# Kernel tuning notes

Hardware: AMD Instinct MI355X
Metric: run time of the kernel (lower is better)

Reference implementation:

```python
import math
import jax, jax.numpy as jnp
import numpy as np

B, S, D = 2, 2048, 512
H = 8
DH = D // H  # 64
FF = 2048


def _uniform(key, shape, c):
    return jax.random.uniform(key, shape, jnp.float32, -c, c)


def setup_inputs() -> dict:
    key = jax.random.key(0)
    ks = jax.random.split(key, 16)
    x = jax.random.normal(ks[0], (B, S, D), jnp.float32)
    c_qkv = math.sqrt(6 / (D + DH))
    wq = _uniform(ks[1], (H, D, DH), c_qkv)
    wk = _uniform(ks[2], (H, D, DH), c_qkv)
    wv = _uniform(ks[3], (H, D, DH), c_qkv)
    bq = jnp.zeros((H, DH), jnp.float32)
    bk = jnp.zeros((H, DH), jnp.float32)
    bv = jnp.zeros((H, DH), jnp.float32)
    c_o = math.sqrt(6 / (H * DH + D))
    wo = _uniform(ks[4], (H * DH, D), c_o)  # stored as (in, out)
    bo = jnp.zeros((D,), jnp.float32)
    gamma1 = jnp.ones((D,), jnp.float32)
    beta1 = jnp.zeros((D,), jnp.float32)
    c_ff = math.sqrt(6 / (D + FF))
    w1 = _uniform(ks[5], (D, FF), c_ff)
    b1 = jnp.zeros((FF,), jnp.float32)
    w2 = _uniform(ks[6], (FF, D), c_ff)
    b2 = jnp.zeros((D,), jnp.float32)
    gamma2 = jnp.ones((D,), jnp.float32)
    beta2 = jnp.zeros((D,), jnp.float32)
    return dict(x=x, wq=wq, bq=bq, wk=wk, bk=bk, wv=wv, bv=bv, wo=wo, bo=bo,
                gamma1=gamma1, beta1=beta1, w1=w1, b1=b1, w2=w2, b2=b2,
                gamma2=gamma2, beta2=beta2)


def _layernorm(x, gamma, beta):
    # matches torch: (x - mean) / std(unbiased=False), no epsilon in denom
    mean = jnp.mean(x, axis=-1, keepdims=True)
    var = jnp.mean((x - mean) ** 2, axis=-1, keepdims=True)
    return gamma * (x - mean) / jnp.sqrt(var) + beta


def reference(x, wq, bq, wk, bk, wv, bv, wo, bo, gamma1, beta1, w1, b1, w2, b2, gamma2, beta2):
    # multi-head attention: all heads batched in one einsum (same math as the per-head loop)
    q = jnp.einsum('bsd,hde->bhse', x, wq) + bq[None, :, None, :]
    k = jnp.einsum('bsd,hde->bhse', x, wk) + bk[None, :, None, :]
    v = jnp.einsum('bsd,hde->bhse', x, wv) + bv[None, :, None, :]
    scores = jnp.einsum('bhse,bhte->bhst', q, k) / math.sqrt(DH)  # [B,H,S,S]
    attn = jax.nn.softmax(scores, axis=-1)
    y = jnp.einsum('bhst,bhte->bhse', attn, v)  # [B,H,S,DH]
    y = y.transpose(0, 2, 1, 3).reshape(B, S, H * DH)
    y = y @ wo + bo
    # residual + LN (dropout is identity in eval)
    y = _layernorm(y + x, gamma1, beta1)
    # feedforward
    f = jax.nn.relu(y @ w1 + b1) @ w2 + b2
    out = _layernorm(f + y, gamma2, beta2)
    return out
```

## Files before the change

### kernel.cpp

```cpp
#include <hip/hip_runtime.h>

typedef __bf16 bf16;
typedef __attribute__((ext_vector_type(8))) __bf16 bf16x8;
typedef __attribute__((ext_vector_type(4))) float f32x4;
typedef __attribute__((ext_vector_type(16))) float f32x16;

#define DEV __device__ __forceinline__

DEV f32x4 mfma16(bf16x8 a, bf16x8 b, f32x4 c) {
  return __builtin_amdgcn_mfma_f32_16x16x32_bf16(a, b, c, 0, 0, 0);
}
DEV f32x16 mfma32(bf16x8 a, bf16x8 b, f32x16 c) {
  return __builtin_amdgcn_mfma_f32_32x32x16_bf16(a, b, c, 0, 0, 0);
}
DEV void gll16(const bf16* g, bf16* l) {
  __builtin_amdgcn_global_load_lds(
      (const __attribute__((address_space(1))) void*)g,
      (__attribute__((address_space(3))) void*)l, 16, 0, 0);
}
DEV unsigned cvtpk(float a, float b) {
  unsigned r;
  asm("v_cvt_pk_bf16_f32 %0, %1, %2" : "=v"(r) : "v"(a), "v"(b));
  return r;
}
DEV void pl32swap(unsigned& x, unsigned& y) {
  asm("v_permlane32_swap_b32 %0, %1" : "+v"(x), "+v"(y));
}

__global__ __launch_bounds__(256) void prep_k(
    const float* __restrict__ x, const float* __restrict__ wq,
    const float* __restrict__ wk, const float* __restrict__ wv,
    const float* __restrict__ wo, const float* __restrict__ w1,
    const float* __restrict__ w2, const float* __restrict__ bq,
    const float* __restrict__ bk, const float* __restrict__ bv,
    bf16* __restrict__ xb, bf16* __restrict__ wqkvT, bf16* __restrict__ woT,
    bf16* __restrict__ w1T, bf16* __restrict__ w2T, float* __restrict__ cb) {
  const int blk = blockIdx.x, tid = threadIdx.x;
  if (blk < 1024) {
    int i = blk * 256 + tid;
    const float4* p = (const float4*)x + (size_t)i * 2;
    float4 a = p[0], b = p[1];
    bf16x8 o;
    o[0] = (bf16)a.x; o[1] = (bf16)a.y; o[2] = (bf16)a.z; o[3] = (bf16)a.w;
    o[4] = (bf16)b.x; o[5] = (bf16)b.y; o[6] = (bf16)b.z; o[7] = (bf16)b.w;
    ((bf16x8*)xb)[i] = o;
    return;
  }
  if (blk == 1792) {
    for (int i = tid; i < 1536; i += 256)
      cb[i] = i < 512 ? bq[i] : (i < 1024 ? bk[i - 512] : bv[i - 1024]);
    return;
  }
  __shared__ float tile[64][65];
  const int t = blk - 1024;
  const float* src;
  bf16* dst;
  int C, Rout, r0, c0;
  if (t < 192) {
    int mat = t / 64, rem = t % 64, head = rem >> 3, rt = rem & 7;
    src = (mat == 0 ? wq : mat == 1 ? wk : wv) + head * 32768;
    dst = wqkvT + (size_t)(mat * 8 + head) * 32768;
    C = 64; Rout = 512; r0 = rt * 64; c0 = 0;
  } else if (t < 256) {
    int t2 = t - 192;
    src = wo; dst = woT; C = 512; Rout = 512;
    r0 = (t2 >> 3) * 64; c0 = (t2 & 7) * 64;
  } else if (t < 512) {
    int t2 = t - 256;
    src = w1; dst = w1T; C = 2048; Rout = 512;
    r0 = (t2 >> 5) * 64; c0 = (t2 & 31) * 64;
  } else {
    int t2 = t - 512;
    src = w2; dst = w2T; C = 512; Rout = 2048;
    r0 = (t2 >> 3) * 64; c0 = (t2 & 7) * 64;
  }
#pragma unroll
  for (int j = 0; j < 4; ++j) {
    int e = j * 256 + tid;
    int r = e >> 4, c4 = e & 15;
    float4 f = *(const float4*)(src + (size_t)(r0 + r) * C + c0 + c4 * 4);
    tile[r][c4 * 4 + 0] = f.x;
    tile[r][c4 * 4 + 1] = f.y;
    tile[r][c4 * 4 + 2] = f.z;
    tile[r][c4 * 4 + 3] = f.w;
  }
  __syncthreads();
  const int co = tid >> 2, rr0 = (tid & 3) * 16;
  bf16x8 o0, o1;
#pragma unroll
  for (int k = 0; k < 8; ++k) o0[k] = (bf16)tile[rr0 + k][co];
#pragma unroll
  for (int k = 0; k < 8; ++k) o1[k] = (bf16)tile[rr0 + 8 + k][co];
  bf16* dp = dst + (size_t)(c0 + co) * Rout + r0 + rr0;
  *(bf16x8*)dp = o0;
  *(bf16x8*)(dp + 8) = o1;
}

__global__ __launch_bounds__(256) void vtrans_k(const bf16* __restrict__ qkv,
                                                bf16* __restrict__ vtb) {
  __shared__ bf16 tile[64 * 68];
  const int tid = threadIdx.x;
  const int s0 = blockIdx.x * 64;
  const int bh = blockIdx.y, b = bh >> 3, hh = bh & 7;
  const bf16* src = qkv + 1024 + hh * 64;
#pragma unroll
  for (int j = 0; j < 2; ++j) {
    int slot = j * 256 + tid;
    int r = slot >> 3, cc = slot & 7;
    *(bf16x8*)(tile + r * 68 + cc * 8) =
        *(const bf16x8*)(src + (size_t)(b * 2048 + s0 + r) * 1536 + cc * 8);
  }
  __syncthreads();
  const int w = tid >> 6, lane = tid & 63;
#pragma unroll
  for (int sb2 = 0; sb2 < 2; ++sb2) {
    int sb = w * 2 + sb2;
    bf16x8 v;
#pragma unroll
    for (int jj = 0; jj < 8; ++jj) v[jj] = tile[(sb * 8 + jj) * 68 + lane];
    *(bf16x8*)(vtb + (size_t)bh * 131072 + (size_t)lane * 2048 + s0 + sb * 8) = v;
  }
}

template <int EPI>
__global__ __launch_bounds__(256) void gemmN64(
    const bf16* __restrict__ A, const bf16* __restrict__ Bt,
    const float* __restrict__ bias, float* __restrict__ outf,
    bf16* __restrict__ outb, int M, int N, int K, int klen) {
  __shared__ bf16 As[128 * 64];
  __shared__ bf16 Bs[64 * 64];
  const int tid = threadIdx.x;
  const int w = tid >> 6, l = tid & 63;
  const int lh = l & 15, lg = l >> 4;
  const int m0 = blockIdx.x * 128, n0 = blockIdx.y * 64;
  const int k0 = blockIdx.z * klen;
  const int mb = (w & 1) * 64, nb = (w >> 1) * 32;
  f32x4 acc[4][2] = {};
  for (int kt = k0; kt < k0 + klen; kt += 64) {
    __syncthreads();
#pragma unroll
    for (int j = 0; j < 4; ++j) {
      int slot = j * 256 + tid;
      int r = slot >> 3, cc = slot & 7;
      int kk = kt + ((cc ^ (r & 7)) << 3);
      gll16(A + (size_t)(m0 + r) * K + kk, As + slot * 8);
    }
#pragma unroll
    for (int j = 0; j < 2; ++j) {
      int slot = j * 256 + tid;
      int r = slot >> 3, cc = slot & 7;
      int kk = kt + ((cc ^ (r & 7)) << 3);
      gll16(Bt + (size_t)(n0 + r) * K + kk, Bs + slot * 8);
    }
    __syncthreads();
#pragma unroll
    for (int kk = 0; kk < 2; ++kk) {
      bf16x8 af[4], bfr[2];
#pragma unroll
      for (int mi = 0; mi < 4; ++mi) {
        int r = mb + mi * 16 + lh;
        af[mi] = *(const bf16x8*)(As + r * 64 + (((kk * 4 + lg) ^ (r & 7)) << 3));
      }
#pragma unroll
      for (int ni = 0; ni < 2; ++ni) {
        int r = nb + ni * 16 + lh;
        bfr[ni] = *(const bf16x8*)(Bs + r * 64 + (((kk * 4 + lg) ^ (r & 7)) << 3));
      }
#pragma unroll
      for (int mi = 0; mi < 4; ++mi)
#pragma unroll
        for (int ni = 0; ni < 2; ++ni)
          acc[mi][ni] = mfma16(af[mi], bfr[ni], acc[mi][ni]);
    }
  }
  float* op = (EPI == 0) ? outf + (size_t)blockIdx.z * M * N : nullptr;
#pragma unroll
  for (int mi = 0; mi < 4; ++mi)
#pragma unroll
    for (int ni = 0; ni < 2; ++ni)
#pragma unroll
      for (int i = 0; i < 4; ++i) {
        int row = m0 + mb + mi * 16 + lg * 4 + i;
        int col = n0 + nb + ni * 16 + lh;
        float v = acc[mi][ni][i];
        if (EPI == 0) {
          op[(size_t)row * N + col] = v;
        } else if (EPI == 1) {
          v += bias[col];
          outb[(size_t)row * N + col] = (bf16)fmaxf(v, 0.f);
        } else {
          v += bias[col];
          outb[(size_t)row * N + col] = (bf16)(col < 512 ? v * 0.125f : v);
        }
      }
}

__global__ __launch_bounds__(512) void attn_fwd2(
    const bf16* __restrict__ qkv,
    const bf16* __restrict__ vtb,
    bf16* __restrict__ Y) {
  __shared__ __align__(16) char lds[65536];
  const int tid = threadIdx.x;
  const int w = tid >> 6, lane = tid & 63;
  const int l31 = lane & 31, h = lane >> 5;
  const int bh = blockIdx.y, b = bh >> 3, hh = bh & 7;
  const int qtile = blockIdx.x;
  const int half = w >> 2, wp = w & 3;
  const int q0 = qtile * 128 + wp * 32;
  const int tl = tid & 255, sh = tid >> 8;

  bf16x8 qf[4];
  {
    const size_t rowQ = (size_t)(b * 2048 + q0 + l31) * 1536 + hh * 64;
#pragma unroll
    for (int g = 0; g < 4; ++g)
      qf[g] = *(const bf16x8*)(qkv + rowQ + g * 16 + h * 8);
  }
  const bf16* Kp = qkv + 512 + hh * 64;
  const bf16* Vp = vtb + (size_t)bh * 131072;

  f32x16 oacc[2] = {};
  float m_run = -1e30f, l_run = 0.f;

#define KBUF(d, hf) ((bf16*)(lds + (d) * 32768 + (hf) * 16384))
#define VBUF(d, hf) ((bf16*)(lds + (d) * 32768 + (hf) * 16384 + 8192))

  auto stage = [&](int i, int d) {
    const int k0 = sh * 1024 + i * 64;
#pragma unroll
    for (int j = 0; j < 2; ++j) {
      int slot = j * 256 + tl;
      int r = slot >> 3, cc = slot & 7;
      gll16(Kp + (size_t)(b * 2048 + k0 + r) * 1536 + ((cc ^ (r & 7)) << 3),
            KBUF(d, sh) + slot * 8);
      gll16(Vp + (size_t)r * 2048 + k0 + ((cc ^ (r & 7)) << 3),
            VBUF(d, sh) + slot * 8);
    }
  };

  stage(0, 0);
  __syncthreads();
  for (int i = 0; i < 16; ++i) {
    const int d = i & 1;
    if (i < 15) stage(i + 1, d ^ 1);
    const bf16* Kt = KBUF(d, half);
    const bf16* Vt = VBUF(d, half);
    f32x16 st[2];
#pragma unroll
    for (int kt = 0; kt < 2; ++kt) {
      f32x16 z = {};
      const int r = kt * 32 + l31;
#pragma unroll
      for (int g = 0; g < 4; ++g) {
        bf16x8 kf = *(const bf16x8*)(Kt + r * 64 + (((2 * g + h) ^ (r & 7)) << 3));
        z = mfma32(kf, qf[g], z);
      }
      st[kt] = z;
    }
    float mx = -1e30f;
#pragma unroll
    for (int kt = 0; kt < 2; ++kt)
#pragma unroll
      for (int r = 0; r < 16; ++r) mx = fmaxf(mx, st[kt][r]);
    mx = fmaxf(mx, __shfl_xor(mx, 32, 64));
    const float m_new = fmaxf(m_run, mx);
    const float scl = __expf(m_run - m_new);
    m_run = m_new;
    float ps = 0.f;
#pragma unroll
    for (int kt = 0; kt < 2; ++kt)
#pragma unroll
      for (int r = 0; r < 16; ++r) {
        float e = __expf(st[kt][r] - m_new);
        st[kt][r] = e;
        ps += e;
      }
    ps += __shfl_xor(ps, 32, 64);
    l_run = l_run * scl + ps;
    oacc[0] = oacc[0] * scl;
    oacc[1] = oacc[1] * scl;
    bf16x8 pf[4];
#pragma unroll
    for (int kt = 0; kt < 2; ++kt)
#pragma unroll
      for (int g = 0; g < 2; ++g) {
        unsigned a0 = cvtpk(st[kt][8 * g + 0], st[kt][8 * g + 1]);
        unsigned a1 = cvtpk(st[kt][8 * g + 2], st[kt][8 * g + 3]);
        unsigned b0 = cvtpk(st[kt][8 * g + 4], st[kt][8 * g + 5]);
        unsigned b1 = cvtpk(st[kt][8 * g + 6], st[kt][8 * g + 7]);
        pl32swap(a0, b0);
        pl32swap(a1, b1);
        union { unsigned u[4]; bf16x8 v; } pk;
        pk.u[0] = a0; pk.u[1] = a1; pk.u[2] = b0; pk.u[3] = b1;
        pf[kt * 2 + g] = pk.v;
      }
#pragma unroll
    for (int t = 0; t < 2; ++t) {
      const int r = t * 32 + l31;
#pragma unroll
      for (int kg = 0; kg < 4; ++kg) {
        bf16x8 vf = *(const bf16x8*)(Vt + r * 64 + (((2 * kg + h) ^ (r & 7)) << 3));
        oacc[t] = mfma32(vf, pf[kg], oacc[t]);
      }
    }
    __syncthreads();
  }

  if (half == 1) {
    char* ob = lds + wp * 8192;
#pragma unroll
    for (int t = 0; t < 2; ++t)
#pragma unroll
      for (int c = 0; c < 4; ++c) {
        f32x4 v4 = {oacc[t][c * 4 + 0], oacc[t][c * 4 + 1],
                    oacc[t][c * 4 + 2], oacc[t][c * 4 + 3]};
        *(f32x4*)(ob + (t * 4 + c) * 1024 + lane * 16) = v4;
      }
    ((float2*)(lds + 32768))[wp * 64 + lane] = make_float2(m_run, l_run);
  }
  __syncthreads();
  bf16* Yt = (bf16*)(lds + 34816);
  if (half == 0) {
    float2 ml2 = ((const float2*)(lds + 32768))[wp * 64 + lane];
    const float mstar = fmaxf(m_run, ml2.x);
    const float e1 = __expf(m_run - mstar), e2 = __expf(ml2.x - mstar);
    const float lstar = l_run * e1 + ml2.y * e2;
    const float r1 = e1 / lstar, r2 = e2 / lstar;
    const char* ob = lds + wp * 8192;
#pragma unroll
    for (int t = 0; t < 2; ++t)
#pragma unroll
      for (int c = 0; c < 4; ++c) {
        f32x4 v4 = *(const f32x4*)(ob + (t * 4 + c) * 1024 + lane * 16);
#pragma unroll
        for (int j = 0; j < 4; ++j)
          oacc[t][c * 4 + j] = oacc[t][c * 4 + j] * r1 + v4[j] * r2;
      }
#pragma unroll
    for (int t = 0; t < 2; ++t)
#pragma unroll
      for (int r = 0; r < 16; ++r) {
        int dh = (r & 3) + 8 * (r >> 2) + 4 * h + 32 * t;
        Yt[(wp * 32 + l31) * 72 + dh] = (bf16)oacc[t][r];
      }
  }
  __syncthreads();
#pragma unroll
  for (int it = 0; it < 2; ++it) {
    int s = it * 512 + tid;
    int ql = s >> 3, cbk = s & 7;
    bf16x8 v = *(const bf16x8*)(Yt + ql * 72 + cbk * 8);
    *(bf16x8*)(Y + (size_t)(b * 2048 + qtile * 128 + ql) * 512 + hh * 64 + cbk * 8) = v;
  }
#undef KBUF
#undef VBUF
}

__global__ __launch_bounds__(256) void add_ln1_k(
    const float* __restrict__ P,
    const float* __restrict__ xres, const float* __restrict__ bias,
    const float* __restrict__ gamma, const float* __restrict__ beta,
    bf16* __restrict__ outb) {
  const int row = blockIdx.x, tid = threadIdx.x;
  const size_t base = (size_t)row * 512;
  const float2 p0 = ((const float2*)(P + base))[tid];
  const float2 p1 = ((const float2*)(P + 2097152 + base))[tid];
  const float2 xr = ((const float2*)(xres + base))[tid];
  const int c = tid * 2;
  float s0 = p0.x + p1.x + bias[c] + xr.x;
  float s1 = p0.y + p1.y + bias[c + 1] + xr.y;
  float sum = s0 + s1;
#pragma unroll
  for (int m = 1; m < 64; m <<= 1) sum += __shfl_xor(sum, m, 64);
  __shared__ float part[4], part2[4];
  const int w = tid >> 6, l = tid & 63;
  if (l == 0) part[w] = sum;
  __syncthreads();
  const float mean = (part[0] + part[1] + part[2] + part[3]) * (1.f / 512.f);
  const float d0 = s0 - mean, d1 = s1 - mean;
  float vs = d0 * d0 + d1 * d1;
#pragma unroll
  for (int m = 1; m < 64; m <<= 1) vs += __shfl_xor(vs, m, 64);
  if (l == 0) part2[w] = vs;
  __syncthreads();
  const float var = (part2[0] + part2[1] + part2[2] + part2[3]) * (1.f / 512.f);
  const float inv = rsqrtf(var);
  outb[base + c] = (bf16)(gamma[c] * (d0 * inv) + beta[c]);
  outb[base + c + 1] = (bf16)(gamma[c + 1] * (d1 * inv) + beta[c + 1]);
}

__global__ __launch_bounds__(256) void add_ln2_k(
    const float* __restrict__ P,
    const bf16* __restrict__ rres, const float* __restrict__ bias,
    const float* __restrict__ gamma, const float* __restrict__ beta,
    float* __restrict__ outf) {
  const int row = blockIdx.x, tid = threadIdx.x;
  const size_t base = (size_t)row * 512;
  const float2 p0 = ((const float2*)(P + base))[tid];
  const float2 p1 = ((const float2*)(P + 2097152 + base))[tid];
  const int c = tid * 2;
  float s0 = p0.x + p1.x + bias[c] + (float)rres[base + c];
  float s1 = p0.y + p1.y + bias[c + 1] + (float)rres[base + c + 1];
  float sum = s0 + s1;
#pragma unroll
  for (int m = 1; m < 64; m <<= 1) sum += __shfl_xor(sum, m, 64);
  __shared__ float part[4], part2[4];
  const int w = tid >> 6, l = tid & 63;
  if (l == 0) part[w] = sum;
  __syncthreads();
  const float mean = (part[0] + part[1] + part[2] + part[3]) * (1.f / 512.f);
  const float d0 = s0 - mean, d1 = s1 - mean;
  float vs = d0 * d0 + d1 * d1;
#pragma unroll
  for (int m = 1; m < 64; m <<= 1) vs += __shfl_xor(vs, m, 64);
  if (l == 0) part2[w] = vs;
  __syncthreads();
  const float var = (part2[0] + part2[1] + part2[2] + part2[3]) * (1.f / 512.f);
  const float inv = rsqrtf(var);
  ((float2*)(outf + base))[tid] =
      make_float2(gamma[c] * (d0 * inv) + beta[c], gamma[c + 1] * (d1 * inv) + beta[c + 1]);
}

extern "C" void kernel_launch(void* const* d_in, const int* in_sizes, int n_in,
                              void* d_out, int out_size, void* d_ws, size_t ws_size,
                              hipStream_t stream) {
  const float* x = (const float*)d_in[0];
  const float* wq = (const float*)d_in[1];
  const float* bq = (const float*)d_in[2];
  const float* wk = (const float*)d_in[3];
  const float* bk = (const float*)d_in[4];
  const float* wv = (const float*)d_in[5];
  const float* bv = (const float*)d_in[6];
  const float* wo = (const float*)d_in[7];
  const float* bo = (const float*)d_in[8];
  const float* g1 = (const float*)d_in[9];
  const float* be1 = (const float*)d_in[10];
  const float* w1 = (const float*)d_in[11];
  const float* b1 = (const float*)d_in[12];
  const float* w2 = (const float*)d_in[13];
  const float* b2 = (const float*)d_in[14];
  const float* g2 = (const float*)d_in[15];
  const float* be2 = (const float*)d_in[16];

  char* ws = (char*)d_ws;
  bf16* xb    = (bf16*)(ws + 0);
  bf16* y1b   = (bf16*)(ws + 0);
  bf16* wqkvT = (bf16*)(ws + 4194304);
  bf16* woT   = (bf16*)(ws + 5767168);
  bf16* w1T   = (bf16*)(ws + 6291456);
  bf16* w2T   = (bf16*)(ws + 8388608);
  float* cb   = (float*)(ws + 10485760);
  bf16* qkvb  = (bf16*)(ws + 10493952);
  float* t0   = (float*)(ws + 10493952);
  bf16* f1    = (bf16*)(ws + 10493952);
  bf16* vtb   = (bf16*)(ws + 23078656);
  bf16* yb    = (bf16*)(ws + 27272960);
  float* f2   = (float*)(ws + 27272960);

  prep_k<<<1793, 256, 0, stream>>>(x, wq, wk, wv, wo, w1, w2, bq, bk, bv,
                                   xb, wqkvT, woT, w1T, w2T, cb);

  gemmN64<2><<<dim3(32, 24, 1), 256, 0, stream>>>(xb, wqkvT, cb, nullptr, qkvb,
                                                  4096, 1536, 512, 512);
  vtrans_k<<<dim3(32, 16), 256, 0, stream>>>(qkvb, vtb);
  attn_fwd2<<<dim3(16, 16), 512, 0, stream>>>(qkvb, vtb, yb);
  gemmN64<0><<<dim3(32, 8, 2), 256, 0, stream>>>(yb, woT, nullptr, t0, nullptr,
                                                 4096, 512, 512, 256);
  add_ln1_k<<<4096, 256, 0, stream>>>(t0, x, bo, g1, be1, y1b);
  gemmN64<1><<<dim3(32, 32, 1), 256, 0, stream>>>(y1b, w1T, b1, nullptr, f1,
                                                  4096, 2048, 512, 512);
  gemmN64<0><<<dim3(32, 8, 2), 256, 0, stream>>>(f1, w2T, nullptr, f2, nullptr,
                                                 4096, 512, 2048, 1024);
  add_ln2_k<<<4096, 256, 0, stream>>>(f2, y1b, b2, g2, be2, (float*)d_out);
}
```

Baseline: 113.4 us.

## Fuse V transpose into QKV GEMM epilogue, use exp2 softmax with lazy rescale

The QKV projection GEMM now writes the V columns straight into the transposed per-head layout, which removes the separate vtrans kernel launch and its extra read and write of V. Q is prescaled by log2(e)/sqrt(64) so the attention softmax can use exp2f. The running max is rescaled only when a tile's max exceeds it by more than 8, which skips most rescale multiplies. s_setprio is raised around the MFMA blocks to favour matrix issue. Risks are strided 8-byte scattered stores in the GEMM epilogue and a larger bounded exponent range in the lazy rescale.

```diff
diff --git a/kernel.cpp b/kernel.cpp
--- a/kernel.cpp
+++ b/kernel.cpp
@@ -1,6 +1,7 @@
 #include <hip/hip_runtime.h>
 
 typedef __bf16 bf16;
+typedef __attribute__((ext_vector_type(4))) __bf16 bf16x4;
 typedef __attribute__((ext_vector_type(8))) __bf16 bf16x8;
 typedef __attribute__((ext_vector_type(4))) float f32x4;
 typedef __attribute__((ext_vector_type(16))) float f32x16;
@@ -26,6 +27,8 @@
 DEV void pl32swap(unsigned& x, unsigned& y) {
   asm("v_permlane32_swap_b32 %0, %1" : "+v"(x), "+v"(y));
 }
+
+#define QSCALE 0.18033688f
 
 __global__ __launch_bounds__(256) void prep_k(
     const float* __restrict__ x, const float* __restrict__ wq,
@@ -96,37 +99,12 @@
   *(bf16x8*)(dp + 8) = o1;
 }
 
-__global__ __launch_bounds__(256) void vtrans_k(const bf16* __restrict__ qkv,
-                                                bf16* __restrict__ vtb) {
-  __shared__ bf16 tile[64 * 68];
-  const int tid = threadIdx.x;
-  const int s0 = blockIdx.x * 64;
-  const int bh = blockIdx.y, b = bh >> 3, hh = bh & 7;
-  const bf16* src = qkv + 1024 + hh * 64;
-#pragma unroll
-  for (int j = 0; j < 2; ++j) {
-    int slot = j * 256 + tid;
-    int r = slot >> 3, cc = slot & 7;
-    *(bf16x8*)(tile + r * 68 + cc * 8) =
-        *(const bf16x8*)(src + (size_t)(b * 2048 + s0 + r) * 1536 + cc * 8);
-  }
-  __syncthreads();
-  const int w = tid >> 6, lane = tid & 63;
-#pragma unroll
-  for (int sb2 = 0; sb2 < 2; ++sb2) {
-    int sb = w * 2 + sb2;
-    bf16x8 v;
-#pragma unroll
-    for (int jj = 0; jj < 8; ++jj) v[jj] = tile[(sb * 8 + jj) * 68 + lane];
-    *(bf16x8*)(vtb + (size_t)bh * 131072 + (size_t)lane * 2048 + s0 + sb * 8) = v;
-  }
-}
-
 template <int EPI>
 __global__ __launch_bounds__(256) void gemmN64(
     const bf16* __restrict__ A, const bf16* __restrict__ Bt,
     const float* __restrict__ bias, float* __restrict__ outf,
-    bf16* __restrict__ outb, int M, int N, int K, int klen) {
+    bf16* __restrict__ outb, bf16* __restrict__ vtb,
+    int M, int N, int K, int klen) {
   __shared__ bf16 As[128 * 64];
   __shared__ bf16 Bs[64 * 64];
   const int tid = threadIdx.x;
@@ -177,11 +155,22 @@
 #pragma unroll
   for (int mi = 0; mi < 4; ++mi)
 #pragma unroll
-    for (int ni = 0; ni < 2; ++ni)
+    for (int ni = 0; ni < 2; ++ni) {
+      const int row0 = m0 + mb + mi * 16 + lg * 4;
+      const int col = n0 + nb + ni * 16 + lh;
+      if (EPI == 2 && col >= 1024) {
+        const int vcol = col - 1024;
+        const int bhv = (row0 >> 11) * 8 + (vcol >> 6);
+        const int dh = vcol & 63, s = row0 & 2047;
+        bf16x4 q4;
+#pragma unroll
+        for (int i = 0; i < 4; ++i) q4[i] = (bf16)(acc[mi][ni][i] + bias[col]);
+        *(bf16x4*)(vtb + (size_t)bhv * 131072 + (size_t)dh * 2048 + s) = q4;
+        continue;
+      }
 #pragma unroll
       for (int i = 0; i < 4; ++i) {
-        int row = m0 + mb + mi * 16 + lg * 4 + i;
-        int col = n0 + nb + ni * 16 + lh;
+        const int row = row0 + i;
         float v = acc[mi][ni][i];
         if (EPI == 0) {
           op[(size_t)row * N + col] = v;
@@ -190,9 +179,10 @@
           outb[(size_t)row * N + col] = (bf16)fmaxf(v, 0.f);
         } else {
           v += bias[col];
-          outb[(size_t)row * N + col] = (bf16)(col < 512 ? v * 0.125f : v);
+          outb[(size_t)row * N + col] = (bf16)(col < 512 ? v * QSCALE : v);
         }
       }
+    }
 }
 
 __global__ __launch_bounds__(512) void attn_fwd2(
@@ -246,6 +236,7 @@
     const bf16* Kt = KBUF(d, half);
     const bf16* Vt = VBUF(d, half);
     f32x16 st[2];
+    __builtin_amdgcn_s_setprio(1);
 #pragma unroll
     for (int kt = 0; kt < 2; ++kt) {
       f32x16 z = {};
@@ -257,28 +248,32 @@
       }
       st[kt] = z;
     }
+    __builtin_amdgcn_s_setprio(0);
     float mx = -1e30f;
 #pragma unroll
     for (int kt = 0; kt < 2; ++kt)
 #pragma unroll
       for (int r = 0; r < 16; ++r) mx = fmaxf(mx, st[kt][r]);
     mx = fmaxf(mx, __shfl_xor(mx, 32, 64));
-    const float m_new = fmaxf(m_run, mx);
-    const float scl = __expf(m_run - m_new);
-    m_run = m_new;
+    if (!__all(mx <= m_run + 8.f)) {
+      const float m_new = fmaxf(m_run, mx);
+      const float scl = exp2f(m_run - m_new);
+      l_run *= scl;
+      oacc[0] = oacc[0] * scl;
+      oacc[1] = oacc[1] * scl;
+      m_run = m_new;
+    }
     float ps = 0.f;
 #pragma unroll
     for (int kt = 0; kt < 2; ++kt)
 #pragma unroll
       for (int r = 0; r < 16; ++r) {
-        float e = __expf(st[kt][r] - m_new);
+        const float e = exp2f(st[kt][r] - m_run);
         st[kt][r] = e;
         ps += e;
       }
     ps += __shfl_xor(ps, 32, 64);
-    l_run = l_run * scl + ps;
-    oacc[0] = oacc[0] * scl;
-    oacc[1] = oacc[1] * scl;
+    l_run += ps;
     bf16x8 pf[4];
 #pragma unroll
     for (int kt = 0; kt < 2; ++kt)
@@ -294,6 +289,7 @@
         pk.u[0] = a0; pk.u[1] = a1; pk.u[2] = b0; pk.u[3] = b1;
         pf[kt * 2 + g] = pk.v;
       }
+    __builtin_amdgcn_s_setprio(1);
 #pragma unroll
     for (int t = 0; t < 2; ++t) {
       const int r = t * 32 + l31;
@@ -303,6 +299,7 @@
         oacc[t] = mfma32(vf, pf[kg], oacc[t]);
       }
     }
+    __builtin_amdgcn_s_setprio(0);
     __syncthreads();
   }
 
@@ -323,7 +320,7 @@
   if (half == 0) {
     float2 ml2 = ((const float2*)(lds + 32768))[wp * 64 + lane];
     const float mstar = fmaxf(m_run, ml2.x);
-    const float e1 = __expf(m_run - mstar), e2 = __expf(ml2.x - mstar);
+    const float e1 = exp2f(m_run - mstar), e2 = exp2f(ml2.x - mstar);
     const float lstar = l_run * e1 + ml2.y * e2;
     const float r1 = e1 / lstar, r2 = e2 / lstar;
     const char* ob = lds + wp * 8192;
@@ -460,16 +457,15 @@
   prep_k<<<1793, 256, 0, stream>>>(x, wq, wk, wv, wo, w1, w2, bq, bk, bv,
                                    xb, wqkvT, woT, w1T, w2T, cb);
 
-  gemmN64<2><<<dim3(32, 24, 1), 256, 0, stream>>>(xb, wqkvT, cb, nullptr, qkvb,
+  gemmN64<2><<<dim3(32, 24, 1), 256, 0, stream>>>(xb, wqkvT, cb, nullptr, qkvb, vtb,
                                                   4096, 1536, 512, 512);
-  vtrans_k<<<dim3(32, 16), 256, 0, stream>>>(qkvb, vtb);
   attn_fwd2<<<dim3(16, 16), 512, 0, stream>>>(qkvb, vtb, yb);
-  gemmN64<0><<<dim3(32, 8, 2), 256, 0, stream>>>(yb, woT, nullptr, t0, nullptr,
+  gemmN64<0><<<dim3(32, 8, 2), 256, 0, stream>>>(yb, woT, nullptr, t0, nullptr, nullptr,
                                                  4096, 512, 512, 256);
   add_ln1_k<<<4096, 256, 0, stream>>>(t0, x, bo, g1, be1, y1b);
-  gemmN64<1><<<dim3(32, 32, 1), 256, 0, stream>>>(y1b, w1T, b1, nullptr, f1,
+  gemmN64<1><<<dim3(32, 32, 1), 256, 0, stream>>>(y1b, w1T, b1, nullptr, f1, nullptr,
                                                   4096, 2048, 512, 512);
-  gemmN64<0><<<dim3(32, 8, 2), 256, 0, stream>>>(f1, w2T, nullptr, f2, nullptr,
+  gemmN64<0><<<dim3(32, 8, 2), 256, 0, stream>>>(f1, w2T, nullptr, f2, nullptr, nullptr,
                                                  4096, 512, 2048, 1024);
   add_ln2_k<<<4096, 256, 0, stream>>>(f2, y1b, b2, g2, be2, (float*)d_out);
 }
```

New measurement: 116.7 us. +2.9%, slower.
